# Kernel tuning notes

Measured on AMD Instinct MI355X. Metric: run time of the kernel, lower is better.

## Reference

```python
import jax, jax.numpy as jnp
import numpy as np

N_HEADS = 16
NOPE = 128
ROPE = 64
VDIM = 128
HEAD_DIM = NOPE + ROPE  # 192


def apply_rope(x, cos, sin):
    # x: [B, S, H, D] with D even; pairs (a, b) rotated by complex freqs.
    B, S, H, D = x.shape
    xr = x.reshape(B, S, H, D // 2, 2)
    a, b = xr[..., 0], xr[..., 1]
    c = cos[None, :, None, :]
    s = sin[None, :, None, :]
    out = jnp.stack([a * c - b * s, a * s + b * c], axis=-1)
    return out.reshape(B, S, H, D)


def setup_inputs() -> dict:
    key = jax.random.key(0)
    ks = jax.random.split(key, 8)
    B, S, DIM = 1, 2048, 2048
    x = jax.random.normal(ks[0], (B, S, DIM), dtype=jnp.float32)
    wq = jax.random.normal(ks[1], (N_HEADS * HEAD_DIM, DIM), dtype=jnp.float32) * (DIM ** -0.5)
    wk = jax.random.normal(ks[2], (N_HEADS * HEAD_DIM, DIM), dtype=jnp.float32) * (DIM ** -0.5)
    wv = jax.random.normal(ks[3], (N_HEADS * VDIM, DIM), dtype=jnp.float32) * (DIM ** -0.5)
    wo = jax.random.normal(ks[4], (DIM, N_HEADS * VDIM), dtype=jnp.float32) * ((N_HEADS * VDIM) ** -0.5)
    # rotary freqs: theta = 10000^{-2i/d}, angles = pos * theta
    inv_freq = 1.0 / (10000.0 ** (np.arange(0, ROPE, 2, dtype=np.float32) / ROPE))
    angles = np.arange(S, dtype=np.float32)[:, None] * inv_freq[None, :]  # [S, 32]
    freqs_cos = jnp.asarray(np.cos(angles))
    freqs_sin = jnp.asarray(np.sin(angles))
    # additive causal mask
    mask = jnp.where(jnp.triu(jnp.ones((S, S), dtype=bool), k=1), -1e9, 0.0).astype(jnp.float32)
    return {"x": x, "wq": wq, "wk": wk, "wv": wv, "wo": wo,
            "freqs_cos": freqs_cos, "freqs_sin": freqs_sin, "mask": mask, "start_pos": 0}


def reference(x, wq, wk, wv, wo, freqs_cos, freqs_sin, mask, start_pos):
    B, S, DIM = x.shape
    q = (x @ wq.T).reshape(B, S, N_HEADS, HEAD_DIM)
    k = (x @ wk.T).reshape(B, S, N_HEADS, HEAD_DIM)
    v = (x @ wv.T).reshape(B, S, N_HEADS, VDIM)
    q_nope, q_pe = q[..., :NOPE], q[..., NOPE:]
    k_nope, k_pe = k[..., :NOPE], k[..., NOPE:]
    q_pe = apply_rope(q_pe, freqs_cos, freqs_sin)
    k_pe = apply_rope(k_pe, freqs_cos, freqs_sin)
    scores = (jnp.einsum('bshd,bthd->bsht', q_nope, k_nope)
              + jnp.einsum('bshd,bthd->bsht', q_pe, k_pe)) * (HEAD_DIM ** -0.5)
    scores = scores + mask[None, :, None, :]
    probs = jax.nn.softmax(scores.astype(jnp.float32), axis=-1).astype(x.dtype)
    out = jnp.einsum('bsht,bthd->bshd', probs, v)
    return out.reshape(B, S, N_HEADS * VDIM) @ wo.T
```

## Files before the change

### kernel.cpp

```cpp
#include <hip/hip_runtime.h>
#include <hip/hip_bf16.h>
#include <math.h>

#define NH 16
#define NOPE 128
#define ROPE 64
#define VDIM 128
#define HD 192
#define SEQ 2048
#define DIM 2048
#define QKD (NH * HD)
#define VD  (NH * VDIM)
#define QKVS 8192

typedef __attribute__((ext_vector_type(8))) short short8;
typedef __attribute__((ext_vector_type(4))) short short4v;
typedef __attribute__((ext_vector_type(4))) float f32x4;
typedef unsigned int u32;

#define WAIT_VM8  0x0F78
#define WAIT_VM6  0x0F76
#define WAIT_VM0  0x0F70
#define WAIT_LGKM 0xC07F

static __device__ inline short f2bf(float f) {
  union { float f; unsigned u; } v; v.f = f;
  unsigned r = (v.u + 0x7fffu + ((v.u >> 16) & 1u)) >> 16;
  return (short)r;
}
static __device__ inline float bf2f(unsigned short u) {
  union { unsigned u; float f; } v; v.u = ((unsigned)u) << 16;
  return v.f;
}

static __device__ __forceinline__ void gload16(const short* g, short* l) {
  __builtin_amdgcn_global_load_lds(
      (const __attribute__((address_space(1))) u32*)g,
      (__attribute__((address_space(3))) u32*)l, 16, 0, 0);
}


#define RDA(pp, hh, mh) do { \
  const char* Lb_ = Lsm + ((pp) * 32768) + ((hh) * 16384) + aoff; \
  afr[0] = *(const short8*)(Lb_ + ((mh) * 4096) + 0); \
  afr[1] = *(const short8*)(Lb_ + ((mh) * 4096) + 1024); \
  afr[2] = *(const short8*)(Lb_ + ((mh) * 4096) + 2048); \
  afr[3] = *(const short8*)(Lb_ + ((mh) * 4096) + 3072); \
} while (0)

#define RDB(pp, hh) do { \
  const char* Lb_ = Lsm + 65536 + ((pp) * 32768) + ((hh) * 16384) + boff; \
  bfr[0] = *(const short8*)(Lb_ + 0); \
  bfr[1] = *(const short8*)(Lb_ + 1024); \
  bfr[2] = *(const short8*)(Lb_ + 2048); \
  bfr[3] = *(const short8*)(Lb_ + 3072); \
} while (0)

#define SA(kt, h) do { \
  char* d_ = Lsm + (((kt) & 1) * 32768) + ((h) * 16384) + wv * 1024; \
  gload16(gA0 + (kt) * 64 + (h) * 32, (short*)d_); \
  gload16(gA1 + (kt) * 64 + (h) * 32, (short*)(d_ + 8192)); \
} while (0)

#define SB(kt, h) do { \
  char* d_ = Lsm + 65536 + (((kt) & 1) * 32768) + ((h) * 16384) + wv * 1024; \
  gload16(gB0 + (kt) * 64 + (h) * 32, (short*)d_); \
  gload16(gB1 + (kt) * 64 + (h) * 32, (short*)(d_ + 8192)); \
} while (0)

#define MFMA1(mi, ni) \
  acc[mi][ni] = __builtin_amdgcn_mfma_f32_16x16x32_bf16(afr[(mi) & 3], bfr[ni], acc[mi][ni], 0, 0, 0)

#define MM(mh) do { \
  MFMA1((mh)*4+0, 0); MFMA1((mh)*4+1, 0); MFMA1((mh)*4+2, 0); MFMA1((mh)*4+3, 0); \
  MFMA1((mh)*4+0, 1); MFMA1((mh)*4+1, 1); MFMA1((mh)*4+2, 1); MFMA1((mh)*4+3, 1); \
  MFMA1((mh)*4+0, 2); MFMA1((mh)*4+1, 2); MFMA1((mh)*4+2, 2); MFMA1((mh)*4+3, 2); \
  MFMA1((mh)*4+0, 3); MFMA1((mh)*4+1, 3); MFMA1((mh)*4+2, 3); MFMA1((mh)*4+3, 3); \
} while (0)

#define GBAR() __builtin_amdgcn_s_barrier()
#define GLGKM0() __builtin_amdgcn_s_waitcnt(WAIT_LGKM)
#define GPRIO1() __builtin_amdgcn_s_setprio(1)
#define GPRIO0() __builtin_amdgcn_s_setprio(0)
#define GNOP ((void)0)

#define TILE(pp, S1, S2, S3, S4, VMW) do { \
  RDA(pp, 0, 0); RDB(pp, 0); S1; \
  GBAR(); GLGKM0(); GPRIO1(); MM(0); GPRIO0(); GBAR(); \
  RDA(pp, 0, 1); S2; \
  GBAR(); GLGKM0(); GPRIO1(); MM(1); GPRIO0(); GBAR(); \
  RDA(pp, 1, 0); RDB(pp, 1); S3; \
  GBAR(); GLGKM0(); GPRIO1(); MM(0); GPRIO0(); GBAR(); \
  RDA(pp, 1, 1); S4; \
  GBAR(); GLGKM0(); GPRIO1(); MM(1); GPRIO0(); VMW; GBAR(); \
} while (0)

__global__ __launch_bounds__(512, 2) void gemm256_bt(
    const short* __restrict__ A, const short* __restrict__ B,
    short* __restrict__ C, int K, int lda, int ldb, int ldc) {
  __shared__ __align__(16) char Lsm[131072];

  const int tid = threadIdx.x;
  const int lane = tid & 63;
  const int l15 = lane & 15;
  const int quad = lane >> 4;
  const int wv = tid >> 6;
  const int wr = wv >> 2, wc = wv & 3;

  const int bid = blockIdx.x;
  const int xcd = bid & 7;
  const int idx = bid >> 3;
  const int m0 = (idx & 7) * 256;
  const int n0 = (xcd * 4 + (idx >> 3)) * 256;

  const short* gA0 = A + (size_t)(m0 + wv * 16 + l15) * lda + quad * 8;
  const short* gA1 = gA0 + (size_t)128 * lda;
  const short* gB0 = B + (size_t)(n0 + wv * 16 + l15) * ldb + quad * 8;
  const short* gB1 = gB0 + (size_t)128 * ldb;

  const int aoff = wr * 8192 + lane * 16;
  const int boff = wc * 4096 + lane * 16;

  f32x4 acc[8][4];
#pragma unroll
  for (int i = 0; i < 8; ++i)
#pragma unroll
    for (int j = 0; j < 4; ++j) acc[i][j] = (f32x4)(0.f);
  short8 afr[4], bfr[4];

  const int NT = K >> 6;

  SB(0, 0); SA(0, 0); SB(0, 1); SA(0, 1);
  SB(1, 0); SA(1, 0); SB(1, 1);
  __builtin_amdgcn_s_waitcnt(WAIT_VM6);
  GBAR();

  int kt = 0;
  for (; kt + 4 <= NT; kt += 2) {
    TILE(0, SA(kt + 1, 1), SB(kt + 2, 0), SA(kt + 2, 0), SB(kt + 2, 1),
         __builtin_amdgcn_s_waitcnt(WAIT_VM6));
    TILE(1, SA(kt + 2, 1), SB(kt + 3, 0), SA(kt + 3, 0), SB(kt + 3, 1),
         __builtin_amdgcn_s_waitcnt(WAIT_VM6));
  }
  TILE(0, SA(kt + 1, 1), GNOP, GNOP, GNOP, __builtin_amdgcn_s_waitcnt(WAIT_VM0));
  TILE(1, GNOP, GNOP, GNOP, GNOP, GNOP);

#pragma unroll
  for (int m = 0; m < 8; ++m) {
    const size_t rb = (size_t)(m0 + wr * 128 + m * 16 + quad * 4) * ldc +
                      n0 + wc * 64 + l15;
#pragma unroll
    for (int n = 0; n < 4; ++n)
#pragma unroll
      for (int r = 0; r < 4; ++r)
        C[rb + (size_t)r * ldc + n * 16] = f2bf(acc[m][n][r]);
  }
}

template <bool BF16OUT>
__global__ __launch_bounds__(256) void gemm_bt(
    const short* __restrict__ A, const short* __restrict__ B,
    void* __restrict__ Cv, int K, int lda, int ldb, int ldc, float oscale) {
  __shared__ __align__(16) short Ls[4][2][4096];

  const int tid = threadIdx.x;
  const int lane = tid & 63;
  const int wave = tid >> 6;
  const int wr = wave >> 1, wc = wave & 1;
  const int lane15 = lane & 15, quad = lane >> 4;
  const int m0 = blockIdx.y * 128, n0 = blockIdx.x * 128;

  const short* gA[4]; const short* gB[4];
#pragma unroll
  for (int i = 0; i < 4; ++i) {
    int gidx = i * 64 + lane;
    int r = gidx >> 2, p = gidx & 3;
    int g = (p ^ ((r >> 1) & 3)) * 8;
    gA[i] = A + (size_t)(m0 + wr * 64 + r) * lda + g;
    gB[i] = B + (size_t)(n0 + wc * 64 + r) * ldb + g;
  }

  f32x4 acc[4][4];
#pragma unroll
  for (int i = 0; i < 4; ++i)
#pragma unroll
    for (int j = 0; j < 4; ++j) acc[i][j] = (f32x4)(0.f);

#pragma unroll
  for (int i = 0; i < 4; ++i) gload16(gA[i], &Ls[wave][0][i * 512]);
#pragma unroll
  for (int i = 0; i < 4; ++i) gload16(gB[i], &Ls[wave][0][2048 + i * 512]);

  const int rsw = (lane15 >> 1) & 3;
  for (int k0 = 0; k0 < K; k0 += 32) {
    const int cur = (k0 >> 5) & 1;
    __builtin_amdgcn_s_waitcnt(WAIT_LGKM);
    if (k0 + 32 < K) {
      const int nxt = cur ^ 1;
#pragma unroll
      for (int i = 0; i < 4; ++i) gload16(gA[i] + k0 + 32, &Ls[wave][nxt][i * 512]);
#pragma unroll
      for (int i = 0; i < 4; ++i) gload16(gB[i] + k0 + 32, &Ls[wave][nxt][2048 + i * 512]);
      __builtin_amdgcn_s_waitcnt(WAIT_VM8);
    } else {
      __builtin_amdgcn_s_waitcnt(WAIT_VM0);
    }
    const short* bufp = &Ls[wave][cur][0];
    short8 af[4], bfv[4];
#pragma unroll
    for (int i = 0; i < 4; ++i)
      af[i] = *(const short8*)&bufp[(i * 16 + lane15) * 32 + (quad ^ rsw) * 8];
#pragma unroll
    for (int j = 0; j < 4; ++j)
      bfv[j] = *(const short8*)&bufp[2048 + (j * 16 + lane15) * 32 + (quad ^ rsw) * 8];
#pragma unroll
    for (int i = 0; i < 4; ++i)
#pragma unroll
      for (int j = 0; j < 4; ++j)
        acc[i][j] = __builtin_amdgcn_mfma_f32_16x16x32_bf16(af[i], bfv[j], acc[i][j], 0, 0, 0);
  }

#pragma unroll
  for (int i = 0; i < 4; ++i)
#pragma unroll
    for (int j = 0; j < 4; ++j)
#pragma unroll
      for (int r = 0; r < 4; ++r) {
        size_t idx = (size_t)(m0 + wr * 64 + i * 16 + quad * 4 + r) * ldc +
                     n0 + wc * 64 + j * 16 + lane15;
        if (BF16OUT)
          ((short*)Cv)[idx] = f2bf(acc[i][j][r] * oscale);
        else
          ((float*)Cv)[idx] = acc[i][j][r];
      }
}

__global__ __launch_bounds__(256) void rope_qk(
    short* __restrict__ qk, const float* __restrict__ cosf, const float* __restrict__ sinf) {
  int idx = blockIdx.x * blockDim.x + threadIdx.x;
  int j = idx & 31;
  int h = (idx >> 5) & (NH - 1);
  int s = idx >> 9;
  if (s >= SEQ) return;

  float c = cosf[s * 32 + j];
  float sn = sinf[s * 32 + j];
  size_t rowb = (size_t)s * QKVS + h * HD + NOPE + 2 * j;

  u32* pq = (u32*)(qk + rowb);
  u32 w = *pq;
  float a = bf2f((unsigned short)(w & 0xffff));
  float b = bf2f((unsigned short)(w >> 16));
  *pq = (u32)(unsigned short)f2bf(a * c - b * sn) |
        ((u32)(unsigned short)f2bf(a * sn + b * c) << 16);

  u32* pk = (u32*)(qk + rowb + QKD);
  w = *pk;
  a = bf2f((unsigned short)(w & 0xffff));
  b = bf2f((unsigned short)(w >> 16));
  *pk = (u32)(unsigned short)f2bf(a * c - b * sn) |
        ((u32)(unsigned short)f2bf(a * sn + b * c) << 16);
}

__global__ __launch_bounds__(256) void bf16_convert(
    const float* __restrict__ in, short* __restrict__ out, int n4) {
  int i = blockIdx.x * 256 + threadIdx.x;
  if (i >= n4) return;
  float4 f = ((const float4*)in)[i];
  short4v o;
  o.x = f2bf(f.x); o.y = f2bf(f.y); o.z = f2bf(f.z); o.w = f2bf(f.w);
  ((short4v*)out)[i] = o;
}

__global__ __launch_bounds__(256) void conv_wqkv(
    const float* __restrict__ wq, const float* __restrict__ wk,
    const float* __restrict__ wv, short* __restrict__ wqkv, int n4) {
  int i = blockIdx.x * 256 + threadIdx.x;
  if (i >= n4) return;
  int row = i >> 9;
  float4 f;
  if (row < QKD) f = ((const float4*)wq)[i];
  else if (row < 2 * QKD) f = ((const float4*)wk)[i - QKD * (DIM / 4)];
  else f = ((const float4*)wv)[i - 2 * QKD * (DIM / 4)];
  short4v o;
  o.x = f2bf(f.x); o.y = f2bf(f.y); o.z = f2bf(f.z); o.w = f2bf(f.w);
  ((short4v*)wqkv)[i] = o;
}

__global__ __launch_bounds__(256) void vt_bf16(
    const short* __restrict__ vb, short* __restrict__ vtb) {
  __shared__ short tile[64][74];
  const int t0 = blockIdx.x * 64;
  const int c0 = blockIdx.y * 64;
  const int tid = threadIdx.x;
#pragma unroll
  for (int i = 0; i < 16; ++i) {
    int idx = i * 256 + tid;
    int r = idx >> 6, c = idx & 63;
    tile[r][c] = vb[(size_t)(t0 + r) * QKVS + c0 + c];
  }
  __syncthreads();
  const int h = c0 >> 7;
  const int dbase = c0 & 127;
#pragma unroll
  for (int i = 0; i < 16; ++i) {
    int idx = i * 256 + tid;
    int d = idx >> 6, t = idx & 63;
    vtb[(size_t)h * VDIM * SEQ + (size_t)(dbase + d) * SEQ + t0 + t] = tile[t][d];
  }
}

#define BQ 128
#define BT 64
#define CHT 8
#define PSTR 76
#define MFIX 8.0f

__global__ __launch_bounds__(512, 4) void attn_part(
    const short* __restrict__ qk,
    const short* __restrict__ vtb,
    short* __restrict__ Opart,
    float* __restrict__ lpart)
{
  __shared__ __align__(16) short Ks[BT * 192];
  __shared__ __align__(16) short Vt[VDIM * BT];
  __shared__ __align__(16) short Ps[8 * 16 * PSTR];

  const int xcd = blockIdx.x;
  const int i0 = blockIdx.y;
  const int h = xcd + ((i0 >= 40) ? 8 : 0);
  int jj = (i0 >= 40) ? (i0 - 40) : i0;
  int qtb = 15;
  while (jj >= (qtb >> 2) + 1) { jj -= (qtb >> 2) + 1; --qtb; }
  const int chk = jj;

  const int tid = threadIdx.x;
  const int wave = tid >> 6;
  const int lane = tid & 63;
  const int lane15 = lane & 15;
  const int quad = lane >> 4;
  const int g = qtb >> 2;
  const int slot = h * 40 + (g + 1) * (2 * g + (qtb & 3)) + chk;
  const int R0 = qtb * BQ;
  const int NT = 2 * qtb + 2;
  const int kt_beg = chk * CHT;
  const int kt_end = min(kt_beg + CHT, NT);
  const float scale = 0.072168784f;

  const int qrow = R0 + wave * 16 + lane15;
  short8 qf[6];
  const short* qbase = qk + (size_t)qrow * QKVS + h * HD + quad * 8;
#pragma unroll
  for (int kc = 0; kc < 6; ++kc) qf[kc] = *(const short8*)(qbase + kc * 32);

  const short* kb = qk + QKD;
  int lKoff[3]; const short* gK[3];
#pragma unroll
  for (int i = 0; i < 3; ++i) {
    int id = i * 512 + tid;
    int row = id / 24, cX = id - row * 24;
    int ch = cX ^ (row & 7);
    lKoff[i] = id * 8;
    gK[i] = kb + (size_t)row * QKVS + h * HD + ch * 8;
  }
  const short* gV[2]; short* lV[2];
#pragma unroll
  for (int i = 0; i < 2; ++i) {
    int id = i * 512 + tid;
    int row = id >> 3, cX = id & 7;
    int ch = cX ^ (row & 7);
    lV[i] = &Vt[id * 8];
    gV[i] = vtb + (size_t)h * VDIM * SEQ + (size_t)row * SEQ + ch * 8;
  }

  f32x4 oacc[8];
#pragma unroll
  for (int i = 0; i < 8; ++i) oacc[i] = (f32x4)(0.f);
  float lsum[4] = {0.f, 0.f, 0.f, 0.f};

  short* pw = &Ps[wave * 16 * PSTR];

  for (int kt = kt_beg; kt < kt_end; ++kt) {
    const int t0 = kt * BT;
    __syncthreads();
#pragma unroll
    for (int i = 0; i < 3; ++i) gload16(gK[i] + (size_t)t0 * QKVS, &Ks[lKoff[i]]);
#pragma unroll
    for (int i = 0; i < 2; ++i) gload16(gV[i] + t0, lV[i]);
    __syncthreads();

    f32x4 sacc[4];
    __builtin_amdgcn_s_setprio(1);
#pragma unroll
    for (int c = 0; c < 4; ++c) {
      sacc[c] = (f32x4)(0.f);
      const int row = c * 16 + lane15;
#pragma unroll
      for (int kc = 0; kc < 6; ++kc) {
        int cX = (4 * kc + quad) ^ (lane15 & 7);
        short8 kf = *(const short8*)&Ks[row * 192 + cX * 8];
        sacc[c] = __builtin_amdgcn_mfma_f32_16x16x32_bf16(qf[kc], kf, sacc[c], 0, 0, 0);
      }
    }
    __builtin_amdgcn_s_setprio(0);

    if (kt >= 2 * qtb) {
#pragma unroll
      for (int c = 0; c < 4; ++c)
#pragma unroll
        for (int r = 0; r < 4; ++r) {
          int tg = t0 + c * 16 + lane15;
          int qg = R0 + wave * 16 + quad * 4 + r;
          if (tg > qg) sacc[c][r] = -1e30f;
        }
    }

#pragma unroll
    for (int c = 0; c < 4; ++c)
#pragma unroll
      for (int r = 0; r < 4; ++r) {
        float p = __expf(sacc[c][r] * scale - MFIX);
        lsum[r] += p;
        pw[(quad * 4 + r) * PSTR + c * 16 + lane15] = f2bf(p);
      }

    short8 pf0 = *(const short8*)&pw[lane15 * PSTR + quad * 8];
    short8 pf1 = *(const short8*)&pw[lane15 * PSTR + 32 + quad * 8];
    __builtin_amdgcn_s_setprio(1);
#pragma unroll
    for (int ch = 0; ch < 8; ++ch) {
      const int row = ch * 16 + lane15;
      int cX0 = quad ^ (lane15 & 7);
      int cX1 = (4 + quad) ^ (lane15 & 7);
      short8 vf0 = *(const short8*)&Vt[row * 64 + cX0 * 8];
      short8 vf1 = *(const short8*)&Vt[row * 64 + cX1 * 8];
      oacc[ch] = __builtin_amdgcn_mfma_f32_16x16x32_bf16(pf0, vf0, oacc[ch], 0, 0, 0);
      oacc[ch] = __builtin_amdgcn_mfma_f32_16x16x32_bf16(pf1, vf1, oacc[ch], 0, 0, 0);
    }
    __builtin_amdgcn_s_setprio(0);
  }

  short* op = Opart + (size_t)slot * (128 * 128);
#pragma unroll
  for (int ch = 0; ch < 8; ++ch)
#pragma unroll
    for (int r = 0; r < 4; ++r)
      op[(wave * 16 + quad * 4 + r) * 128 + ch * 16 + lane15] = f2bf(oacc[ch][r]);

  float red[4];
#pragma unroll
  for (int r = 0; r < 4; ++r) {
    float s = lsum[r];
    s += __shfl_xor(s, 1, 64);
    s += __shfl_xor(s, 2, 64);
    s += __shfl_xor(s, 4, 64);
    s += __shfl_xor(s, 8, 64);
    red[r] = s;
  }
  if (lane15 == 0) {
#pragma unroll
    for (int r = 0; r < 4; ++r)
      lpart[(size_t)slot * 128 + wave * 16 + quad * 4 + r] = red[r];
  }
}

__global__ __launch_bounds__(256) void attn_combine(
    const short* __restrict__ Opart, const float* __restrict__ lpart,
    short* __restrict__ aob) {
  const int qt64 = blockIdx.x, h = blockIdx.y;
  const int qtb = qt64 >> 1;
  const int half = qt64 & 1;
  const int g = qtb >> 2;
  const int nact = g + 1;
  const int base = h * 40 + (g + 1) * (2 * g + (qtb & 3));
  const int tid = threadIdx.x;
  const int row = tid >> 2;
  const int cg = (tid & 3) * 32;

  float acc[32];
#pragma unroll
  for (int e = 0; e < 32; ++e) acc[e] = 0.f;
  float lsum = 0.f;

  for (int c = 0; c < nact; ++c) {
    const short* sp = Opart + (size_t)(base + c) * (128 * 128) +
                      (half * 64 + row) * 128 + cg;
    lsum += lpart[(size_t)(base + c) * 128 + half * 64 + row];
#pragma unroll
    for (int gg = 0; gg < 4; ++gg) {
      short8 vv = *(const short8*)(sp + gg * 8);
#pragma unroll
      for (int e = 0; e < 8; ++e) acc[gg * 8 + e] += bf2f((unsigned short)vv[e]);
    }
  }

  float inv = 1.f / lsum;
#pragma unroll
  for (int gg = 0; gg < 4; ++gg) {
    short8 ov;
#pragma unroll
    for (int e = 0; e < 8; ++e) ov[e] = f2bf(acc[gg * 8 + e] * inv);
    *(short8*)(aob + (size_t)(qt64 * 64 + row) * QKVS + h * 128 + cg + gg * 8) = ov;
  }
}

extern "C" void kernel_launch(void* const* d_in, const int* in_sizes, int n_in,
                              void* d_out, int out_size, void* d_ws, size_t ws_size,
                              hipStream_t stream) {
  const float* x  = (const float*)d_in[0];
  const float* wq = (const float*)d_in[1];
  const float* wk = (const float*)d_in[2];
  const float* wv = (const float*)d_in[3];
  const float* wo = (const float*)d_in[4];
  const float* fc = (const float*)d_in[5];
  const float* fs = (const float*)d_in[6];

  char* ws8 = (char*)d_ws;
  short* xb    = (short*)(ws8 + 0);
  short* wo_b  = (short*)(ws8 + 0);
  short* wqkv  = (short*)(ws8 + 8388608);
  short* vtb   = (short*)(ws8 + 8388608);
  short* Opart = (short*)(ws8 + 16777216);
  float* lpart = (float*)(ws8 + 37748736);
  short* qkv   = (short*)(ws8 + 41943040);
  float* out   = (float*)d_out;

  const int NX4 = DIM * DIM / 4;
  const int NQKV4 = QKVS * DIM / 4;
  const int ROPE_GRID = (SEQ * NH * 32) / 256;

  bf16_convert<<<(NX4 + 255) / 256, 256, 0, stream>>>(x, xb, NX4);
  conv_wqkv<<<(NQKV4 + 255) / 256, 256, 0, stream>>>(wq, wk, wv, wqkv, NQKV4);

  gemm256_bt<<<dim3((QKVS / 256) * (SEQ / 256)), 512, 0, stream>>>(
      xb, wqkv, qkv, DIM, DIM, DIM, QKVS);
  rope_qk<<<ROPE_GRID, 256, 0, stream>>>(qkv, fc, fs);
  vt_bf16<<<dim3(SEQ / 64, VD / 64), 256, 0, stream>>>(qkv + 2 * QKD, vtb);

  bf16_convert<<<(NX4 + 255) / 256, 256, 0, stream>>>(wo, wo_b, NX4);

  attn_part<<<dim3(8, 80), 512, 0, stream>>>(qkv, vtb, Opart, lpart);
  attn_combine<<<dim3(SEQ / 64, NH), 256, 0, stream>>>(Opart, lpart, qkv + 2 * QKD);

  gemm_bt<false><<<dim3(DIM / 128, SEQ / 128), 256, 0, stream>>>(
      qkv + 2 * QKD, wo_b, out, DIM, QKVS, DIM, DIM, 1.0f);
}
```

Baseline: 324.9 us.

## Restructure 256-tile GEMM main loop into two half-K phases with wider fragment loads

The 256x256 bf16 GEMM now loads all eight A fragments and four B fragments per half-K step and issues 32 MFMAs between barriers, where it used to issue four 16-MFMA phases per tile. Global-to-LDS prefetches are reordered so both A and B halves are fetched together, and the vmcnt waits are retuned to match. The goal is fewer barriers and waitcnt stalls per k-tile and longer uninterrupted MFMA runs. The cost is more VGPRs for the larger A fragment array, which could pressure occupancy at launch bounds 512x2, and prefetch now starts later relative to compute.

```diff
diff --git a/kernel.cpp b/kernel.cpp
--- a/kernel.cpp
+++ b/kernel.cpp
@@ -20,6 +20,7 @@
 
 #define WAIT_VM8  0x0F78
 #define WAIT_VM6  0x0F76
+#define WAIT_VM4  0x0F74
 #define WAIT_VM0  0x0F70
 #define WAIT_LGKM 0xC07F
 
@@ -42,10 +43,10 @@
 
 #define RDA(pp, hh, mh) do { \
   const char* Lb_ = Lsm + ((pp) * 32768) + ((hh) * 16384) + aoff; \
-  afr[0] = *(const short8*)(Lb_ + ((mh) * 4096) + 0); \
-  afr[1] = *(const short8*)(Lb_ + ((mh) * 4096) + 1024); \
-  afr[2] = *(const short8*)(Lb_ + ((mh) * 4096) + 2048); \
-  afr[3] = *(const short8*)(Lb_ + ((mh) * 4096) + 3072); \
+  afr[(mh) * 4 + 0] = *(const short8*)(Lb_ + ((mh) * 4096) + 0); \
+  afr[(mh) * 4 + 1] = *(const short8*)(Lb_ + ((mh) * 4096) + 1024); \
+  afr[(mh) * 4 + 2] = *(const short8*)(Lb_ + ((mh) * 4096) + 2048); \
+  afr[(mh) * 4 + 3] = *(const short8*)(Lb_ + ((mh) * 4096) + 3072); \
 } while (0)
 
 #define RDB(pp, hh) do { \
@@ -69,13 +70,17 @@
 } while (0)
 
 #define MFMA1(mi, ni) \
-  acc[mi][ni] = __builtin_amdgcn_mfma_f32_16x16x32_bf16(afr[(mi) & 3], bfr[ni], acc[mi][ni], 0, 0, 0)
-
-#define MM(mh) do { \
-  MFMA1((mh)*4+0, 0); MFMA1((mh)*4+1, 0); MFMA1((mh)*4+2, 0); MFMA1((mh)*4+3, 0); \
-  MFMA1((mh)*4+0, 1); MFMA1((mh)*4+1, 1); MFMA1((mh)*4+2, 1); MFMA1((mh)*4+3, 1); \
-  MFMA1((mh)*4+0, 2); MFMA1((mh)*4+1, 2); MFMA1((mh)*4+2, 2); MFMA1((mh)*4+3, 2); \
-  MFMA1((mh)*4+0, 3); MFMA1((mh)*4+1, 3); MFMA1((mh)*4+2, 3); MFMA1((mh)*4+3, 3); \
+  acc[mi][ni] = __builtin_amdgcn_mfma_f32_16x16x32_bf16(afr[mi], bfr[ni], acc[mi][ni], 0, 0, 0)
+
+#define MM2() do { \
+  MFMA1(0,0); MFMA1(1,0); MFMA1(2,0); MFMA1(3,0); \
+  MFMA1(4,0); MFMA1(5,0); MFMA1(6,0); MFMA1(7,0); \
+  MFMA1(0,1); MFMA1(1,1); MFMA1(2,1); MFMA1(3,1); \
+  MFMA1(4,1); MFMA1(5,1); MFMA1(6,1); MFMA1(7,1); \
+  MFMA1(0,2); MFMA1(1,2); MFMA1(2,2); MFMA1(3,2); \
+  MFMA1(4,2); MFMA1(5,2); MFMA1(6,2); MFMA1(7,2); \
+  MFMA1(0,3); MFMA1(1,3); MFMA1(2,3); MFMA1(3,3); \
+  MFMA1(4,3); MFMA1(5,3); MFMA1(6,3); MFMA1(7,3); \
 } while (0)
 
 #define GBAR() __builtin_amdgcn_s_barrier()
@@ -84,15 +89,11 @@
 #define GPRIO0() __builtin_amdgcn_s_setprio(0)
 #define GNOP ((void)0)
 
-#define TILE(pp, S1, S2, S3, S4, VMW) do { \
-  RDA(pp, 0, 0); RDB(pp, 0); S1; \
-  GBAR(); GLGKM0(); GPRIO1(); MM(0); GPRIO0(); GBAR(); \
-  RDA(pp, 0, 1); S2; \
-  GBAR(); GLGKM0(); GPRIO1(); MM(1); GPRIO0(); GBAR(); \
-  RDA(pp, 1, 0); RDB(pp, 1); S3; \
-  GBAR(); GLGKM0(); GPRIO1(); MM(0); GPRIO0(); GBAR(); \
-  RDA(pp, 1, 1); S4; \
-  GBAR(); GLGKM0(); GPRIO1(); MM(1); GPRIO0(); VMW; GBAR(); \
+#define TILE2(pp, S1, S2, W1, S3, S4, W2) do { \
+  RDA(pp, 0, 0); RDA(pp, 0, 1); RDB(pp, 0); S1; S2; \
+  GBAR(); GLGKM0(); GPRIO1(); MM2(); GPRIO0(); W1; GBAR(); \
+  RDA(pp, 1, 0); RDA(pp, 1, 1); RDB(pp, 1); S3; S4; \
+  GBAR(); GLGKM0(); GPRIO1(); MM2(); GPRIO0(); W2; GBAR(); \
 } while (0)
 
 __global__ __launch_bounds__(512, 2) void gemm256_bt(
@@ -126,24 +127,26 @@
   for (int i = 0; i < 8; ++i)
 #pragma unroll
     for (int j = 0; j < 4; ++j) acc[i][j] = (f32x4)(0.f);
-  short8 afr[4], bfr[4];
+  short8 afr[8], bfr[4];
 
   const int NT = K >> 6;
 
-  SB(0, 0); SA(0, 0); SB(0, 1); SA(0, 1);
-  SB(1, 0); SA(1, 0); SB(1, 1);
-  __builtin_amdgcn_s_waitcnt(WAIT_VM6);
+  SA(0, 0); SB(0, 0); SA(0, 1); SB(0, 1);
+  SA(1, 0); SB(1, 0);
+  __builtin_amdgcn_s_waitcnt(WAIT_VM8);
   GBAR();
 
   int kt = 0;
   for (; kt + 4 <= NT; kt += 2) {
-    TILE(0, SA(kt + 1, 1), SB(kt + 2, 0), SA(kt + 2, 0), SB(kt + 2, 1),
-         __builtin_amdgcn_s_waitcnt(WAIT_VM6));
-    TILE(1, SA(kt + 2, 1), SB(kt + 3, 0), SA(kt + 3, 0), SB(kt + 3, 1),
-         __builtin_amdgcn_s_waitcnt(WAIT_VM6));
-  }
-  TILE(0, SA(kt + 1, 1), GNOP, GNOP, GNOP, __builtin_amdgcn_s_waitcnt(WAIT_VM0));
-  TILE(1, GNOP, GNOP, GNOP, GNOP, GNOP);
+    TILE2(0, SA(kt + 1, 1), SB(kt + 1, 1), __builtin_amdgcn_s_waitcnt(WAIT_VM8),
+             SA(kt + 2, 0), SB(kt + 2, 0), __builtin_amdgcn_s_waitcnt(WAIT_VM8));
+    TILE2(1, SA(kt + 2, 1), SB(kt + 2, 1), __builtin_amdgcn_s_waitcnt(WAIT_VM8),
+             SA(kt + 3, 0), SB(kt + 3, 0), __builtin_amdgcn_s_waitcnt(WAIT_VM8));
+  }
+  TILE2(0, SA(kt + 1, 1), SB(kt + 1, 1), __builtin_amdgcn_s_waitcnt(WAIT_VM8),
+           GNOP, GNOP, __builtin_amdgcn_s_waitcnt(WAIT_VM4));
+  TILE2(1, GNOP, GNOP, __builtin_amdgcn_s_waitcnt(WAIT_VM0),
+           GNOP, GNOP, GNOP);
 
 #pragma unroll
   for (int m = 0; m < 8; ++m) {
```

Result: no change. 326.9 us (+0.6%).

## Switch 256x256 GEMM LDS layout to row-major XOR-swizzled tiles with regrouped prefetch

Applied to the files above, without the earlier changes.

Changes the shared-memory tile layout of the 256x256 bf16 GEMM from split-K halves to full 64-wide rows with an XOR swizzle on the column chunk. Global-to-LDS loads are reorganized into two groups per k-tile, and A fragments are kept in eight registers instead of being reloaded. The aim is to cut LDS bank conflicts and get more coalesced global row reads. In exchange it uses more VGPRs and changes the wait counts and prefetch timing.

```diff
diff --git a/kernel.cpp b/kernel.cpp
--- a/kernel.cpp
+++ b/kernel.cpp
@@ -20,6 +20,7 @@
 
 #define WAIT_VM8  0x0F78
 #define WAIT_VM6  0x0F76
+#define WAIT_VM4  0x0F74
 #define WAIT_VM0  0x0F70
 #define WAIT_LGKM 0xC07F
 
@@ -40,36 +41,32 @@
 }
 
 
-#define RDA(pp, hh, mh) do { \
-  const char* Lb_ = Lsm + ((pp) * 32768) + ((hh) * 16384) + aoff; \
-  afr[0] = *(const short8*)(Lb_ + ((mh) * 4096) + 0); \
-  afr[1] = *(const short8*)(Lb_ + ((mh) * 4096) + 1024); \
-  afr[2] = *(const short8*)(Lb_ + ((mh) * 4096) + 2048); \
-  afr[3] = *(const short8*)(Lb_ + ((mh) * 4096) + 3072); \
+#define LSA(pp) (Lsm + (pp) * 65536)
+#define LSB(pp) (Lsm + (pp) * 65536 + 32768)
+
+#define RDA(pp, kh, mh) do { \
+  const char* p_ = LSA(pp) + abase + (mh) * 8192 + ((kh) ? cx1 : cx0); \
+  afr[(mh) * 4 + 0] = *(const short8*)(p_ + 0); \
+  afr[(mh) * 4 + 1] = *(const short8*)(p_ + 2048); \
+  afr[(mh) * 4 + 2] = *(const short8*)(p_ + 4096); \
+  afr[(mh) * 4 + 3] = *(const short8*)(p_ + 6144); \
 } while (0)
 
-#define RDB(pp, hh) do { \
-  const char* Lb_ = Lsm + 65536 + ((pp) * 32768) + ((hh) * 16384) + boff; \
-  bfr[0] = *(const short8*)(Lb_ + 0); \
-  bfr[1] = *(const short8*)(Lb_ + 1024); \
-  bfr[2] = *(const short8*)(Lb_ + 2048); \
-  bfr[3] = *(const short8*)(Lb_ + 3072); \
+#define RDB(pp, kh) do { \
+  const char* p_ = LSB(pp) + bbase + ((kh) ? cx1 : cx0); \
+  bfr[0] = *(const short8*)(p_ + 0); \
+  bfr[1] = *(const short8*)(p_ + 2048); \
+  bfr[2] = *(const short8*)(p_ + 4096); \
+  bfr[3] = *(const short8*)(p_ + 6144); \
 } while (0)
 
-#define SA(kt, h) do { \
-  char* d_ = Lsm + (((kt) & 1) * 32768) + ((h) * 16384) + wv * 1024; \
-  gload16(gA0 + (kt) * 64 + (h) * 32, (short*)d_); \
-  gload16(gA1 + (kt) * 64 + (h) * 32, (short*)(d_ + 8192)); \
-} while (0)
-
-#define SB(kt, h) do { \
-  char* d_ = Lsm + 65536 + (((kt) & 1) * 32768) + ((h) * 16384) + wv * 1024; \
-  gload16(gB0 + (kt) * 64 + (h) * 32, (short*)d_); \
-  gload16(gB1 + (kt) * 64 + (h) * 32, (short*)(d_ + 8192)); \
-} while (0)
+#define SGA(kt, c) gload16(srcA[c] + (kt) * 64, (short*)(LSA((kt) & 1) + ((c) * 512 + tid) * 16))
+#define SGB(kt, c) gload16(srcB[c] + (kt) * 64, (short*)(LSB((kt) & 1) + ((c) * 512 + tid) * 16))
+#define G1S(kt) do { SGA(kt, 0); SGA(kt, 2); SGB(kt, 0); SGB(kt, 1); } while (0)
+#define G2S(kt) do { SGA(kt, 1); SGA(kt, 3); SGB(kt, 2); SGB(kt, 3); } while (0)
 
 #define MFMA1(mi, ni) \
-  acc[mi][ni] = __builtin_amdgcn_mfma_f32_16x16x32_bf16(afr[(mi) & 3], bfr[ni], acc[mi][ni], 0, 0, 0)
+  acc[mi][ni] = __builtin_amdgcn_mfma_f32_16x16x32_bf16(afr[mi], bfr[ni], acc[mi][ni], 0, 0, 0)
 
 #define MM(mh) do { \
   MFMA1((mh)*4+0, 0); MFMA1((mh)*4+1, 0); MFMA1((mh)*4+2, 0); MFMA1((mh)*4+3, 0); \
@@ -84,14 +81,14 @@
 #define GPRIO0() __builtin_amdgcn_s_setprio(0)
 #define GNOP ((void)0)
 
-#define TILE(pp, S1, S2, S3, S4, VMW) do { \
-  RDA(pp, 0, 0); RDB(pp, 0); S1; \
+#define TILE(pp, SP1, SP4, VMW) do { \
+  RDA(pp, 0, 0); RDB(pp, 0); SP1; \
   GBAR(); GLGKM0(); GPRIO1(); MM(0); GPRIO0(); GBAR(); \
-  RDA(pp, 0, 1); S2; \
+  RDA(pp, 0, 1); \
   GBAR(); GLGKM0(); GPRIO1(); MM(1); GPRIO0(); GBAR(); \
-  RDA(pp, 1, 0); RDB(pp, 1); S3; \
+  RDA(pp, 1, 0); RDB(pp, 1); \
   GBAR(); GLGKM0(); GPRIO1(); MM(0); GPRIO0(); GBAR(); \
-  RDA(pp, 1, 1); S4; \
+  RDA(pp, 1, 1); SP4; \
   GBAR(); GLGKM0(); GPRIO1(); MM(1); GPRIO0(); VMW; GBAR(); \
 } while (0)
 
@@ -113,37 +110,40 @@
   const int m0 = (idx & 7) * 256;
   const int n0 = (xcd * 4 + (idx >> 3)) * 256;
 
-  const short* gA0 = A + (size_t)(m0 + wv * 16 + l15) * lda + quad * 8;
-  const short* gA1 = gA0 + (size_t)128 * lda;
-  const short* gB0 = B + (size_t)(n0 + wv * 16 + l15) * ldb + quad * 8;
-  const short* gB1 = gB0 + (size_t)128 * ldb;
-
-  const int aoff = wr * 8192 + lane * 16;
-  const int boff = wc * 4096 + lane * 16;
+  const int trow = tid >> 3;
+  const int scol = ((tid & 7) * 8) ^ ((trow & 7) * 8);
+  const short* srcA[4]; const short* srcB[4];
+#pragma unroll
+  for (int c = 0; c < 4; ++c) {
+    srcA[c] = A + (size_t)(m0 + c * 64 + trow) * lda + scol;
+    srcB[c] = B + (size_t)(n0 + c * 64 + trow) * ldb + scol;
+  }
+
+  const int abase = (wr * 128 + l15) * 128;
+  const int bbase = (wc * 64 + l15) * 128;
+  const int cx0 = (quad * 16) ^ ((l15 & 7) * 16);
+  const int cx1 = (64 + quad * 16) ^ ((l15 & 7) * 16);
 
   f32x4 acc[8][4];
 #pragma unroll
   for (int i = 0; i < 8; ++i)
 #pragma unroll
     for (int j = 0; j < 4; ++j) acc[i][j] = (f32x4)(0.f);
-  short8 afr[4], bfr[4];
+  short8 afr[8], bfr[4];
 
   const int NT = K >> 6;
 
-  SB(0, 0); SA(0, 0); SB(0, 1); SA(0, 1);
-  SB(1, 0); SA(1, 0); SB(1, 1);
-  __builtin_amdgcn_s_waitcnt(WAIT_VM6);
+  G1S(0); G2S(0); G1S(1);
+  __builtin_amdgcn_s_waitcnt(WAIT_VM4);
   GBAR();
 
   int kt = 0;
   for (; kt + 4 <= NT; kt += 2) {
-    TILE(0, SA(kt + 1, 1), SB(kt + 2, 0), SA(kt + 2, 0), SB(kt + 2, 1),
-         __builtin_amdgcn_s_waitcnt(WAIT_VM6));
-    TILE(1, SA(kt + 2, 1), SB(kt + 3, 0), SA(kt + 3, 0), SB(kt + 3, 1),
-         __builtin_amdgcn_s_waitcnt(WAIT_VM6));
-  }
-  TILE(0, SA(kt + 1, 1), GNOP, GNOP, GNOP, __builtin_amdgcn_s_waitcnt(WAIT_VM0));
-  TILE(1, GNOP, GNOP, GNOP, GNOP, GNOP);
+    TILE(0, G2S(kt + 1), G1S(kt + 2), __builtin_amdgcn_s_waitcnt(WAIT_VM4));
+    TILE(1, G2S(kt + 2), G1S(kt + 3), __builtin_amdgcn_s_waitcnt(WAIT_VM4));
+  }
+  TILE(0, G2S(kt + 1), GNOP, __builtin_amdgcn_s_waitcnt(WAIT_VM0));
+  TILE(1, GNOP, GNOP, GNOP);
 
 #pragma unroll
   for (int m = 0; m < 8; ++m) {
```

Measured after the change: 314.5 us. -3.2%, faster.
